# Kernel optimization log

Measured on AMD Instinct MI355X. Metric: run time of the kernel, lower is better.

The kernel has to match this reference:

```python
import jax, jax.numpy as jnp
import numpy as np

LAMBDA_SOFTMAX = 9.0
LAMBDA_LSE = 6.0
MARGIN = 0.2
EPS = 1e-8


def setup_inputs() -> dict:
    key = jax.random.key(0)
    k1, k2, k3 = jax.random.split(key, 3)
    Ni, R, W, d = 128, 36, 50, 1024
    im = jax.random.normal(k1, (Ni, R, d), dtype=jnp.float32)
    s = jax.random.normal(k2, (Ni, W, d), dtype=jnp.float32)
    s_l = jax.random.randint(k3, (Ni,), 5, W + 1, dtype=jnp.int32)
    return {"im": im, "s": s, "s_l": s_l}


def _scan_t2i_scores(im, s, s_l):
    # im: (Ni, R, d) images; s: (Nc, W, d) captions; s_l: (Nc,) caption lengths
    Nc, W, _ = s.shape
    word_mask = jnp.arange(W)[None, :] < s_l[:, None]          # (Nc, W)
    # attn[c,i,r,w] = <im[i,r], s[c,w]>  (bmm(context, query^T) per caption)
    attn = jnp.einsum('ird,cwd->cirw', im, s)                  # (Nc, Ni, R, W)
    # clipped_l2norm: LeakyReLU(0.1) then l2-normalize over word dim
    attn = jax.nn.leaky_relu(attn, 0.1)
    attn = attn * word_mask[:, None, None, :]                  # zero padded words
    norm = jnp.sqrt(jnp.sum(attn * attn, axis=3, keepdims=True)) + EPS
    attn = attn / norm
    # transpose to (Nc, Ni, W, R), smooth-softmax over regions
    attn_t = jax.nn.softmax(jnp.swapaxes(attn, 2, 3) * LAMBDA_SOFTMAX, axis=-1)
    # weighted image context per word: (Nc, Ni, W, d)
    wei = jnp.einsum('ird,ciwr->ciwd', im, attn_t)
    # cosine similarity along d between cap word and weighted context
    w12 = jnp.einsum('cwd,ciwd->ciw', s, wei)                  # (Nc, Ni, W)
    w1 = jnp.linalg.norm(s, axis=-1)                           # (Nc, W)
    w2 = jnp.linalg.norm(wei, axis=-1)                         # (Nc, Ni, W)
    row_sim = w12 / jnp.clip(w1[:, None, :] * w2, EPS, None)
    # LogSumExp aggregation over valid words only
    e = jnp.where(word_mask[:, None, :], jnp.exp(row_sim * LAMBDA_LSE), 0.0)
    sims = jnp.log(jnp.sum(e, axis=2)) / LAMBDA_LSE            # (Nc, Ni)
    return sims.T                                              # scores[i, c]


def reference(im, s, s_l) -> jnp.ndarray:
    scores = _scan_t2i_scores(im, s, s_l)                      # (Ni, Nc), Ni == Nc
    diag = jnp.diag(scores)[:, None]
    cost_s = jnp.clip(MARGIN + scores - diag, 0.0, None)       # caption retrieval
    cost_im = jnp.clip(MARGIN + scores - diag.T, 0.0, None)    # image retrieval
    eye = jnp.eye(scores.shape[0], dtype=bool)
    cost_s = jnp.where(eye, 0.0, cost_s)
    cost_im = jnp.where(eye, 0.0, cost_im)
    # max_violation=True: hardest negative per row/column
    return jnp.max(cost_s, axis=1).sum() + jnp.max(cost_im, axis=0).sum()
```

## Files before the change

kernel.cpp:

```cpp
#include <hip/hip_runtime.h>
#include <hip/hip_bf16.h>
#include <cstdint>

using u16 = unsigned short;
using u32 = unsigned int;
using bf16x8 = __attribute__((ext_vector_type(8))) short;
using f32x4  = __attribute__((ext_vector_type(4))) float;

#define NI 128
#define NC 128
#define RR 36
#define WW 50
#define DD 1024
#define LDC 6400
#define ATS 37
#define IMN ((size_t)NI * RR * DD)
#define SN  ((size_t)NC * WW * DD)

#define GLL16(g, l) __builtin_amdgcn_global_load_lds(                        \
    (const __attribute__((address_space(1))) void*)(g),                      \
    (__attribute__((address_space(3))) void*)(l), 16, 0, 0)

typedef const __attribute__((address_space(4))) float cfloat;

__device__ __forceinline__ float2 bf16pair(u32 u) {
  float2 f;
  f.x = __uint_as_float(u << 16);
  f.y = __uint_as_float(u & 0xffff0000u);
  return f;
}

__device__ __forceinline__ u32 bf16_rne(u32 x) {
  return (x + 0x7FFFu + ((x >> 16) & 1u)) >> 16;
}

__global__ __launch_bounds__(256) void convert_in(const void* __restrict__ im_in,
                                                  const void* __restrict__ s_in,
                                                  u16* __restrict__ imB,
                                                  u16* __restrict__ sB,
                                                  int* __restrict__ flag) {
  __shared__ int cnt;
  if (threadIdx.x == 0) cnt = 0;
  __syncthreads();
  const u16* imu = (const u16*)im_in;
  int local = 0;
#pragma unroll
  for (int v = 0; v < 16; ++v) {
    u16 u = imu[threadIdx.x * 16 + v];
    if (((u >> 7) & 0xFF) >= 0xC0) local++;
  }
  if (local) atomicAdd(&cnt, local);
  __syncthreads();
  const int f = (cnt > 4) ? 1 : 0;
  if (blockIdx.x == 0 && threadIdx.x == 0) *flag = f;
  if (!f) return;

  const size_t TOT8 = (IMN + SN) / 8;
  const size_t stride = (size_t)gridDim.x * blockDim.x;
  for (size_t g = (size_t)blockIdx.x * blockDim.x + threadIdx.x; g < TOT8; g += stride) {
    size_t base = g * 8;
    const u32* sp;
    u16* dst;
    if (base < IMN) { sp = (const u32*)im_in + base; dst = imB + base; }
    else            { sp = (const u32*)s_in + (base - IMN); dst = sB + (base - IMN); }
    u16 o[8];
#pragma unroll
    for (int e = 0; e < 8; ++e) o[e] = (u16)bf16_rne(sp[e]);
    *(uint4*)dst = *(const uint4*)o;
  }
}

__global__ __launch_bounds__(256) void gram_w1(const u16* __restrict__ im_orig,
                                               const u16* __restrict__ im_conv,
                                               const u16* __restrict__ s_orig,
                                               const u16* __restrict__ s_conv,
                                               const int* __restrict__ flag,
                                               float* __restrict__ G,
                                               float* __restrict__ w1) {
  const u16* im = *flag ? im_conv : im_orig;
  const u16* s  = *flag ? s_conv : s_orig;
  __shared__ u16 ims[48 * 520];
  const int b = blockIdx.x;
  const int t = threadIdx.x;
  const int lane = t & 63, wv = t >> 6;
  const int lm = lane & 15, q = lane >> 4;
  f32x4 acc[3][3] = {};

  for (int p = 0; p < 2; ++p) {
    const int kk = p * 512;
#pragma unroll
    for (int v = 0; v < 9; ++v) {
      int u = t + v * 256;
      int row = u >> 6;
      int kloc = (u & 63) * 8;
      uint4 val = *(const uint4*)(im + (size_t)b * (RR * DD) + (size_t)row * DD + kk + kloc);
      *(uint4*)&ims[row * 520 + kloc] = val;
    }
    if (p == 0) {
#pragma unroll
      for (int v = 0; v < 4; ++v) {
        int u = t + v * 256;
        if (u < 780) {
          uint4 z; z.x = 0; z.y = 0; z.z = 0; z.w = 0;
          *(uint4*)&ims[36 * 520 + u * 8] = z;
        }
      }
    }
    __syncthreads();
#pragma unroll
    for (int kq = 0; kq < 4; ++kq) {
      const int ks = wv * 4 + kq;
      bf16x8 af[3];
#pragma unroll
      for (int mi = 0; mi < 3; ++mi)
        af[mi] = *(const bf16x8*)&ims[(mi * 16 + lm) * 520 + ks * 32 + q * 8];
#pragma unroll
      for (int mi = 0; mi < 3; ++mi)
#pragma unroll
        for (int ni = 0; ni < 3; ++ni)
          acc[mi][ni] = __builtin_amdgcn_mfma_f32_16x16x32_bf16(af[mi], af[ni], acc[mi][ni], 0, 0, 0);
    }
    __syncthreads();
  }
  float* red = (float*)ims;
  if (wv > 0) {
#pragma unroll
    for (int mi = 0; mi < 3; ++mi)
#pragma unroll
      for (int ni = 0; ni < 3; ++ni)
#pragma unroll
        for (int v = 0; v < 4; ++v) {
          int row = mi * 16 + q * 4 + v;
          int col = ni * 16 + lm;
          red[(wv - 1) * 2304 + row * 48 + col] = acc[mi][ni][v];
        }
  }
  __syncthreads();
  if (wv == 0) {
#pragma unroll
    for (int mi = 0; mi < 3; ++mi)
#pragma unroll
      for (int ni = 0; ni < 3; ++ni)
#pragma unroll
        for (int v = 0; v < 4; ++v) {
          int row = mi * 16 + q * 4 + v;
          int col = ni * 16 + lm;
          float r0 = acc[mi][ni][v] + red[row * 48 + col] +
                     red[2304 + row * 48 + col] + red[4608 + row * 48 + col];
          if (row < RR && col < RR)
            G[(size_t)b * (RR * RR) + row * RR + col] = r0;
        }
  }
  const u16* sc = s + (size_t)b * WW * DD;
  for (int w = wv; w < WW; w += 4) {
    const u16* sp = sc + (size_t)w * DD + lane * 16;
    uint4 A0 = *(const uint4*)sp;
    uint4 A1 = *(const uint4*)(sp + 8);
    float sum = 0.f;
    u32 uu[8] = {A0.x, A0.y, A0.z, A0.w, A1.x, A1.y, A1.z, A1.w};
#pragma unroll
    for (int e = 0; e < 8; ++e) {
      float2 f = bf16pair(uu[e]);
      sum += f.x * f.x + f.y * f.y;
    }
#pragma unroll
    for (int off = 32; off > 0; off >>= 1) sum += __shfl_down(sum, off);
    if (lane == 0) w1[b * WW + w] = sqrtf(sum);
  }
}

__global__ __launch_bounds__(256) void gemm_raw(const u16* __restrict__ A_orig,
                                                const u16* __restrict__ A_conv,
                                                const u16* __restrict__ B_orig,
                                                const u16* __restrict__ B_conv,
                                                const int* __restrict__ flag,
                                                u16* __restrict__ C) {
  const u16* A = *flag ? A_conv : A_orig;
  const u16* B = *flag ? B_conv : B_orig;
  __shared__ u16 As[128 * 64];
  __shared__ u16 Bs[128 * 64];
  const int t = threadIdx.x;
  const int col0 = blockIdx.x * 128;
  const int row0 = blockIdx.y * 128;
  const int lane = t & 63, wv = t >> 6;
  const int wm = wv >> 1, wn = wv & 1;
  const int lm = lane & 15, q = lane >> 4;
  f32x4 acc[4][4] = {};

  const u16* ap[4];
  const u16* bp[4];
#pragma unroll
  for (int v = 0; v < 4; ++v) {
    int u = t + v * 256;
    int row = u >> 3;
    int c = (u & 7) ^ (row & 7);
    ap[v] = A + (size_t)(row0 + row) * DD + c * 8;
    bp[v] = B + (size_t)(col0 + row) * DD + c * 8;
  }

  for (int k0 = 0; k0 < DD; k0 += 64) {
#pragma unroll
    for (int v = 0; v < 4; ++v) GLL16(ap[v] + k0, &As[(t + v * 256) * 8]);
#pragma unroll
    for (int v = 0; v < 4; ++v) GLL16(bp[v] + k0, &Bs[(t + v * 256) * 8]);
    __syncthreads();
#pragma unroll
    for (int ks = 0; ks < 2; ++ks) {
      bf16x8 af[4], bf[4];
      const int pch = (ks * 4 + q) ^ (lm & 7);
#pragma unroll
      for (int mi = 0; mi < 4; ++mi)
        af[mi] = *(const bf16x8*)&As[(wm * 64 + mi * 16 + lm) * 64 + pch * 8];
#pragma unroll
      for (int ni = 0; ni < 4; ++ni)
        bf[ni] = *(const bf16x8*)&Bs[(wn * 64 + ni * 16 + lm) * 64 + pch * 8];
#pragma unroll
      for (int mi = 0; mi < 4; ++mi)
#pragma unroll
        for (int ni = 0; ni < 4; ++ni)
          acc[mi][ni] = __builtin_amdgcn_mfma_f32_16x16x32_bf16(af[mi], bf[ni], acc[mi][ni], 0, 0, 0);
    }
    __syncthreads();
  }
#pragma unroll
  for (int mi = 0; mi < 4; ++mi)
#pragma unroll
    for (int ni = 0; ni < 4; ++ni)
#pragma unroll
      for (int v = 0; v < 4; ++v) {
        int rr = row0 + wm * 64 + mi * 16 + q * 4 + v;
        int cc = col0 + wn * 64 + ni * 16 + lm;
        C[(size_t)rr * LDC + cc] = (u16)bf16_rne(__float_as_uint(acc[mi][ni][v]));
      }
}

__global__ __launch_bounds__(256, 2) void postproc(const u16* __restrict__ raw,
                                                   const float* __restrict__ G,
                                                   const float* __restrict__ w1,
                                                   const int* __restrict__ s_l,
                                                   float* __restrict__ scores) {
  const int i = blockIdx.y;
  const int wv = threadIdx.x >> 6;
  const int c = blockIdx.x * 4 + wv;
  const int lane = threadIdx.x & 63;
  __shared__ float aT[4][WW * ATS];
  __shared__ float nrm9_s[4][RR];
  const int L = s_l[c];

  if (lane < RR) {
    const u16* rp = raw + (size_t)(i * RR + lane) * LDC + c * WW;
    float sum = 0.f;
#pragma unroll
    for (int j = 0; j < 25; ++j) {
      float2 v = bf16pair(((const u32*)rp)[j]);
      float x0 = v.x > 0.f ? v.x : 0.1f * v.x;
      float x1 = v.y > 0.f ? v.y : 0.1f * v.y;
      if (2 * j     >= L) x0 = 0.f;
      if (2 * j + 1 >= L) x1 = 0.f;
      aT[wv][(2 * j) * ATS + lane]     = x0;
      aT[wv][(2 * j + 1) * ATS + lane] = x1;
      sum += x0 * x0 + x1 * x1;
    }
    nrm9_s[wv][lane] = 9.0f / (sqrtf(sum) + 1e-8f);
  }
  __syncthreads();

  const int wIdx = lane < WW ? lane : WW - 1;
  const float* row = &aT[wv][wIdx * ATS];
  cfloat* Gp = (cfloat*)(G + (size_t)i * (RR * RR));

  float x[RR];
  float m = -1e30f;
#pragma unroll
  for (int r = 0; r < RR; ++r) {
    x[r] = row[r];
    m = fmaxf(m, x[r] * nrm9_s[wv][r]);
  }
  float e[RR];
  float sum = 0.f, w12r = 0.f;
#pragma unroll
  for (int r = 0; r < RR; ++r) {
    float er = __expf(x[r] * nrm9_s[wv][r] - m);
    e[r] = er;
    sum += er;
    w12r += er * (x[r] > 0.f ? x[r] : 10.0f * x[r]);
  }
  float qq2 = 0.f;
#pragma unroll
  for (int r = 0; r < RR; ++r) {
    float h = 0.5f * Gp[r * RR + r] * e[r];
#pragma unroll
    for (int j = r + 1; j < RR; ++j)
      h += Gp[r * RR + j] * e[j];
    qq2 += e[r] * h;
  }
  float qq = 2.0f * qq2;
  float w1v = w1[c * WW + wIdx];
  float denom = fmaxf(w1v * sqrtf(fmaxf(qq, 0.f)), 1e-8f * sum);
  float rs = w12r / denom;
  float ew = (lane < L) ? __expf(6.0f * rs) : 0.f;
#pragma unroll
  for (int off = 32; off > 0; off >>= 1) ew += __shfl_down(ew, off);
  if (lane == 0) scores[i * NC + c] = logf(ew) * (1.0f / 6.0f);
}

__global__ __launch_bounds__(128) void loss_k(const float* __restrict__ scores,
                                              u32* __restrict__ out) {
  __shared__ float diag[NI];
  __shared__ float red[NI];
  const int t = threadIdx.x;
  diag[t] = scores[t * NC + t];
  __syncthreads();
  const float di = diag[t];
  float rowmax = 0.f, colmax = 0.f;
  for (int k = 0; k < NC; ++k) {
    if (k != t) {
      float sr = scores[t * NC + k];
      rowmax = fmaxf(rowmax, fmaxf(0.2f + sr - di, 0.f));
      float sc = scores[k * NC + t];
      colmax = fmaxf(colmax, fmaxf(0.2f + sc - di, 0.f));
    }
  }
  red[t] = rowmax + colmax;
  __syncthreads();
  for (int st = 64; st > 0; st >>= 1) {
    if (t < st) red[t] += red[t + st];
    __syncthreads();
  }
  if (t == 0) {
    u32 b = bf16_rne(__float_as_uint(red[0]));
    out[0] = b | (b << 16);
  }
}

extern "C" void kernel_launch(void* const* d_in, const int* in_sizes, int n_in,
                              void* d_out, int out_size, void* d_ws, size_t ws_size,
                              hipStream_t stream) {
  const void* im_in = d_in[0];
  const void* s_in  = d_in[1];
  const int*  sl    = (const int*)d_in[2];

  char* ws = (char*)d_ws;
  u16*   imB    = (u16*)ws;
  u16*   sB     = (u16*)(ws + 9437184);
  u16*   raw    = (u16*)(ws + 22544384);
  float* G      = (float*)(ws + 22544384 + 58982400);
  float* w1     = G + 128 * RR * RR;
  float* scores = w1 + NC * WW;
  int*   flag   = (int*)(scores + NI * NC);

  convert_in<<<dim3(2048), dim3(256), 0, stream>>>(im_in, s_in, imB, sB, flag);
  gram_w1<<<dim3(128), dim3(256), 0, stream>>>((const u16*)im_in, imB,
                                               (const u16*)s_in, sB, flag, G, w1);
  gemm_raw<<<dim3(50, 36), dim3(256), 0, stream>>>((const u16*)im_in, imB,
                                                   (const u16*)s_in, sB, flag, raw);
  postproc<<<dim3(32, 128), dim3(256), 0, stream>>>(raw, G, w1, sl, scores);
  loss_k<<<dim3(1), dim3(128), 0, stream>>>(scores, (u32*)d_out);
}
```

Measured before the change: 281.3 us.

## Rewrite GEMM with 256x256 tiles, 4-stage LDS ring, and XCD-aware block mapping

The bf16 GEMM that builds the raw attention matrix now uses 512-thread blocks computing 256x256 output tiles. Operands stream through a 4-deep ring of 32-wide K slices, with async global-to-LDS loads issued three stages ahead and explicit vmcnt waits plus barriers, so loads overlap MFMA work. A 1D grid of 450 blocks is remapped so each XCD gets a contiguous set of tiles, improving L2 locality. It also raises MFMA priority around compute and changes the LDS swizzle, at the cost of more registers per thread and more LDS per block.

```diff
diff --git a/kernel.cpp b/kernel.cpp
--- a/kernel.cpp
+++ b/kernel.cpp
@@ -169,66 +169,108 @@
   }
 }
 
-__global__ __launch_bounds__(256) void gemm_raw(const u16* __restrict__ A_orig,
-                                                const u16* __restrict__ A_conv,
-                                                const u16* __restrict__ B_orig,
-                                                const u16* __restrict__ B_conv,
-                                                const int* __restrict__ flag,
-                                                u16* __restrict__ C) {
+#define STAGE(koff, SD)                                                      \
+  do {                                                                       \
+    GLL16(aP0 + (koff), &ringA[SD][t * 8]);                                  \
+    GLL16(aP1 + (koff), &ringA[SD][t * 8 + 4096]);                           \
+    GLL16(bP0 + (koff), &ringB[SD][t * 8]);                                  \
+    GLL16(bP1 + (koff), &ringB[SD][t * 8 + 4096]);                           \
+  } while (0)
+
+#define PHASE(S)                                                             \
+  do {                                                                       \
+    bf16x8 af[8], bf[4];                                                     \
+    _Pragma("unroll")                                                        \
+    for (int mi = 0; mi < 8; ++mi)                                           \
+      af[mi] = *(const bf16x8*)&ringA[S][aBase + mi * 512];                  \
+    _Pragma("unroll")                                                        \
+    for (int ni = 0; ni < 4; ++ni)                                           \
+      bf[ni] = *(const bf16x8*)&ringB[S][bBase + ni * 512];                  \
+    __builtin_amdgcn_s_setprio(1);                                           \
+    _Pragma("unroll")                                                        \
+    for (int mi = 0; mi < 8; ++mi)                                           \
+      _Pragma("unroll")                                                      \
+      for (int ni = 0; ni < 4; ++ni)                                         \
+        acc[mi][ni] = __builtin_amdgcn_mfma_f32_16x16x32_bf16(               \
+            af[mi], bf[ni], acc[mi][ni], 0, 0, 0);                           \
+    __builtin_amdgcn_s_setprio(0);                                           \
+  } while (0)
+
+#define WAIT_BAR(N)                                                          \
+  do {                                                                       \
+    asm volatile("s_waitcnt vmcnt(" #N ")" ::: "memory");                    \
+    __builtin_amdgcn_s_barrier();                                            \
+    asm volatile("" ::: "memory");                                           \
+  } while (0)
+
+__global__ __launch_bounds__(512, 2) void gemm_raw(const u16* __restrict__ A_orig,
+                                                   const u16* __restrict__ A_conv,
+                                                   const u16* __restrict__ B_orig,
+                                                   const u16* __restrict__ B_conv,
+                                                   const int* __restrict__ flag,
+                                                   u16* __restrict__ C) {
   const u16* A = *flag ? A_conv : A_orig;
   const u16* B = *flag ? B_conv : B_orig;
-  __shared__ u16 As[128 * 64];
-  __shared__ u16 Bs[128 * 64];
+  __shared__ u16 ringA[4][8192];
+  __shared__ u16 ringB[4][8192];
   const int t = threadIdx.x;
-  const int col0 = blockIdx.x * 128;
-  const int row0 = blockIdx.y * 128;
+
+  const int orig = blockIdx.x;
+  const int xcd = orig & 7, jb = orig >> 3;
+  const int wg = (xcd < 2 ? xcd * 57 : 114 + (xcd - 2) * 56) + jb;
+  const int tm = wg / 25;
+  const int tn = wg - tm * 25;
+  const int row0 = tm * 256, col0 = tn * 256;
+
   const int lane = t & 63, wv = t >> 6;
-  const int wm = wv >> 1, wn = wv & 1;
+  const int wm = wv >> 2, wn = wv & 3;
   const int lm = lane & 15, q = lane >> 4;
-  f32x4 acc[4][4] = {};
-
-  const u16* ap[4];
-  const u16* bp[4];
-#pragma unroll
-  for (int v = 0; v < 4; ++v) {
-    int u = t + v * 256;
-    int row = u >> 3;
-    int c = (u & 7) ^ (row & 7);
-    ap[v] = A + (size_t)(row0 + row) * DD + c * 8;
-    bp[v] = B + (size_t)(col0 + row) * DD + c * 8;
-  }
-
-  for (int k0 = 0; k0 < DD; k0 += 64) {
-#pragma unroll
-    for (int v = 0; v < 4; ++v) GLL16(ap[v] + k0, &As[(t + v * 256) * 8]);
-#pragma unroll
-    for (int v = 0; v < 4; ++v) GLL16(bp[v] + k0, &Bs[(t + v * 256) * 8]);
-    __syncthreads();
-#pragma unroll
-    for (int ks = 0; ks < 2; ++ks) {
-      bf16x8 af[4], bf[4];
-      const int pch = (ks * 4 + q) ^ (lm & 7);
-#pragma unroll
-      for (int mi = 0; mi < 4; ++mi)
-        af[mi] = *(const bf16x8*)&As[(wm * 64 + mi * 16 + lm) * 64 + pch * 8];
-#pragma unroll
-      for (int ni = 0; ni < 4; ++ni)
-        bf[ni] = *(const bf16x8*)&Bs[(wn * 64 + ni * 16 + lm) * 64 + pch * 8];
-#pragma unroll
-      for (int mi = 0; mi < 4; ++mi)
-#pragma unroll
-        for (int ni = 0; ni < 4; ++ni)
-          acc[mi][ni] = __builtin_amdgcn_mfma_f32_16x16x32_bf16(af[mi], bf[ni], acc[mi][ni], 0, 0, 0);
-    }
-    __syncthreads();
-  }
-#pragma unroll
-  for (int mi = 0; mi < 4; ++mi)
+  const int chunk = (lm & 1) * 4 + (q ^ ((lm >> 1) & 3));
+  const int aBase = (wm * 64 + (lm >> 1)) * 64 + chunk * 8;
+  const int bBase = (wn * 32 + (lm >> 1)) * 64 + chunk * 8;
+
+  const int i0 = t, i1 = t + 512;
+  const int r0s = (i0 >> 3) * 2 + ((i0 & 7) >> 2);
+  const int r1s = (i1 >> 3) * 2 + ((i1 & 7) >> 2);
+  const int lc0 = (i0 & 3) ^ ((i0 >> 3) & 3);
+  const int lc1 = (i1 & 3) ^ ((i1 >> 3) & 3);
+  const u16* aP0 = A + (size_t)(row0 + r0s) * DD + lc0 * 8;
+  const u16* aP1 = A + (size_t)(row0 + r1s) * DD + lc1 * 8;
+  const u16* bP0 = B + (size_t)(col0 + r0s) * DD + lc0 * 8;
+  const u16* bP1 = B + (size_t)(col0 + r1s) * DD + lc1 * 8;
+
+  f32x4 acc[8][4] = {};
+
+  STAGE(0, 0);
+  STAGE(32, 1);
+  STAGE(64, 2);
+  WAIT_BAR(8);
+
+  for (int k4 = 0; k4 < 7; ++k4) {
+    const int kb = k4 * 128 + 96;
+#pragma unroll
+    for (int j = 0; j < 4; ++j) {
+      STAGE(kb + j * 32, ((j + 3) & 3));
+      PHASE(j);
+      WAIT_BAR(8);
+    }
+  }
+  STAGE(992, 3);
+  PHASE(0);
+  WAIT_BAR(8);
+  PHASE(1);
+  WAIT_BAR(4);
+  PHASE(2);
+  WAIT_BAR(0);
+  PHASE(3);
+
+#pragma unroll
+  for (int mi = 0; mi < 8; ++mi)
 #pragma unroll
     for (int ni = 0; ni < 4; ++ni)
 #pragma unroll
       for (int v = 0; v < 4; ++v) {
-        int rr = row0 + wm * 64 + mi * 16 + q * 4 + v;
+        int rr = row0 + wm * 128 + mi * 16 + q * 4 + v;
         int cc = col0 + wn * 64 + ni * 16 + lm;
         C[(size_t)rr * LDC + cc] = (u16)bf16_rne(__float_as_uint(acc[mi][ni][v]));
       }
@@ -352,8 +394,8 @@
   convert_in<<<dim3(2048), dim3(256), 0, stream>>>(im_in, s_in, imB, sB, flag);
   gram_w1<<<dim3(128), dim3(256), 0, stream>>>((const u16*)im_in, imB,
                                                (const u16*)s_in, sB, flag, G, w1);
-  gemm_raw<<<dim3(50, 36), dim3(256), 0, stream>>>((const u16*)im_in, imB,
-                                                   (const u16*)s_in, sB, flag, raw);
+  gemm_raw<<<dim3(450), dim3(512), 0, stream>>>((const u16*)im_in, imB,
+                                                (const u16*)s_in, sB, flag, raw);
   postproc<<<dim3(32, 128), dim3(256), 0, stream>>>(raw, G, w1, sl, scores);
   loss_k<<<dim3(1), dim3(128), 0, stream>>>(scores, (u32*)d_out);
 }
```

Result: faster. 270.9 us (-3.7%).
